# Kernel optimization log

Measured on AMD Instinct MI355X. Metric: run time of the kernel, lower is better.

Reference implementation:

```python
import jax, jax.numpy as jnp
import numpy as np

DEPTH, HEADS, DIM_HEAD = 6, 8, 64
B, N, E = 2, 128, 160
NUM_ATOMS, NF = 100, 127
DIM = NF + 1                 # 128, node feature dim fed to transformer
INNER = HEADS * DIM_HEAD     # 512


def setup_inputs() -> dict:
    key = jax.random.key(0)
    ks = iter(jax.random.split(key, 40))
    f32 = jnp.float32
    def w(shape, scale=0.02):
        return jax.random.normal(next(ks), shape, dtype=f32) * scale
    inp = {
        "indices": jax.random.randint(next(ks), (B, N), 0, NUM_ATOMS),
        "coordinates": jax.random.normal(next(ks), (B, N, 3), dtype=f32),
        "bonds": jax.random.randint(next(ks), (E, 2), 0, N),
        "noise_level": jax.random.uniform(next(ks), (1,), dtype=f32),
        "atom_emb": w((NUM_ATOMS, NF), 1.0),
        "ln1_g": jnp.ones((DEPTH, DIM), f32), "ln1_b": jnp.zeros((DEPTH, DIM), f32),
        "Wq": w((DEPTH, DIM, INNER)), "bq": jnp.zeros((DEPTH, INNER), f32),
        "Wkv": w((DEPTH, DIM, 2 * INNER)), "bkv": jnp.zeros((DEPTH, 2 * INNER), f32),
        "We": w((DEPTH, 3, INNER)), "be": jnp.zeros((DEPTH, INNER), f32),
        "Wo": w((DEPTH, INNER, DIM)), "bo": jnp.zeros((DEPTH, DIM), f32),
        "Wg1": w((DEPTH, 3 * DIM, 1)),
        "ln2_g": jnp.ones((DEPTH, DIM), f32), "ln2_b": jnp.zeros((DEPTH, DIM), f32),
        "W1": w((DEPTH, DIM, 4 * DIM)), "b1": jnp.zeros((DEPTH, 4 * DIM), f32),
        "W2": w((DEPTH, 4 * DIM, DIM)), "b2": jnp.zeros((DEPTH, DIM), f32),
        "Wg2": w((DEPTH, 3 * DIM, 1)),
        "Wlin": w((DIM, 1)), "blin": jnp.zeros((1,), f32),
    }
    return inp


def _ln(x, g, b, eps=1e-5):
    m = jnp.mean(x, -1, keepdims=True)
    v = jnp.mean((x - m) ** 2, -1, keepdims=True)
    return (x - m) * jax.lax.rsqrt(v + eps) * g + b


def _gated_residual(x, res, Wg):
    # gate = sigmoid(Linear([x, res, x-res])); out = x*gate + res*(1-gate)
    gate = jax.nn.sigmoid(jnp.concatenate([x, res, x - res], -1) @ Wg)  # (B,N,1)
    return x * gate + res * (1.0 - gate)


def _forward(indices, bonds, coordinates, noise_level, atom_emb,
             ln1_g, ln1_b, Wq, bq, Wkv, bkv, We, be, Wo, bo, Wg1,
             ln2_g, ln2_b, W1, b1, W2, b2, Wg2, Wlin, blin):
    b, n = indices.shape
    # nodes_embedding: atom embedding + noise-level channel
    noise = jnp.broadcast_to(noise_level.reshape(1, 1, 1).astype(coordinates.dtype), (b, n, 1))
    nodes = jnp.concatenate([atom_emb[indices], noise], -1)  # (B,N,DIM)
    # edges_embedding: vectorized scatter of per-bond coordinate differences
    i, j = bonds[:, 0], bonds[:, 1]
    diff = coordinates[:, i] - coordinates[:, j]             # (B,E,3)
    edges = jnp.zeros((b, n, n, 3), coordinates.dtype)
    edges = edges.at[:, i, j].set(diff).at[:, j, i].set(-diff)

    scale = DIM_HEAD ** -0.5
    for l in range(DEPTH):
        # PreNorm + edge-biased attention (mask is all-ones -> no-op)
        xn = _ln(nodes, ln1_g[l], ln1_b[l])
        q = (xn @ Wq[l] + bq[l]).reshape(b, n, HEADS, DIM_HEAD)
        k, v = jnp.split(xn @ Wkv[l] + bkv[l], 2, -1)
        k = k.reshape(b, n, HEADS, DIM_HEAD)
        v = v.reshape(b, n, HEADS, DIM_HEAD)
        e = (edges @ We[l] + be[l]).reshape(b, n, n, HEADS, DIM_HEAD)
        kk = k[:, None] + e                                   # (B,i,j,H,D)
        vv = v[:, None] + e
        sim = jnp.einsum('bihd,bijhd->bijh', q, kk) * scale
        attn = jax.nn.softmax(sim, axis=2)                    # softmax over j
        out = jnp.einsum('bijh,bijhd->bihd', attn, vv).reshape(b, n, INNER)
        out = out @ Wo[l] + bo[l]
        nodes = _gated_residual(out, nodes, Wg1[l])
        # PreNorm + FeedForward (exact GELU, mult=4) + gated residual
        xn = _ln(nodes, ln2_g[l], ln2_b[l])
        ff = jax.nn.gelu(xn @ W1[l] + b1[l], approximate=False) @ W2[l] + b2[l]
        nodes = _gated_residual(ff, nodes, Wg2[l])
    return jnp.sum(nodes @ Wlin + blin)


def reference(indices, coordinates, bonds, noise_level, atom_emb,
              ln1_g, ln1_b, Wq, bq, Wkv, bkv, We, be, Wo, bo, Wg1,
              ln2_g, ln2_b, W1, b1, W2, b2, Wg2, Wlin, blin):
    return _forward(indices, bonds, coordinates, noise_level, atom_emb,
                    ln1_g, ln1_b, Wq, bq, Wkv, bkv, We, be, Wo, bo, Wg1,
                    ln2_g, ln2_b, W1, b1, W2, b2, Wg2, Wlin, blin)
```

## Files before the change

### kernel.cpp

```cpp
#include <hip/hip_runtime.h>
#include <hip/hip_fp16.h>
#include <math.h>

#define DEPTH 6
#define HEADS 8
#define BB    2
#define NN    128
#define EE    160
#define NF    127
#define DIMM  128
#define INNER 512
#define NNODE 256

__device__ __forceinline__ void gload16(const void* g, void* l) {
    __builtin_amdgcn_global_load_lds((const __attribute__((address_space(1))) void*)g,
                                     (__attribute__((address_space(3))) void*)l,
                                     16, 0, 0);
}

__device__ __forceinline__ void wait_vm0() { __builtin_amdgcn_s_waitcnt(0x0f70); }
__device__ __forceinline__ void wait_lgkm0() { __builtin_amdgcn_s_waitcnt(0xC07F); }

__device__ __forceinline__ void wstage16(const char* gslice, char* ldsslice, int ln) {
#pragma unroll
    for (int i = 0; i < 16; i++)
        gload16(gslice + i * 1024 + ln * 16, ldsslice + i * 1024);
}
__device__ __forceinline__ void wstage16s(const char* gslice, int rowstride,
                                          char* ldsslice, int ln) {
#pragma unroll
    for (int i = 0; i < 16; i++)
        gload16(gslice + (size_t)i * rowstride + ln * 16, ldsslice + i * 1024);
}

__device__ __forceinline__ void fma8h(float4& a0, float4& a1, float s, float4 raw) {
    const __half2* hp = (const __half2*)&raw;
    float2 p0 = __half22float2(hp[0]), p1 = __half22float2(hp[1]);
    float2 p2 = __half22float2(hp[2]), p3 = __half22float2(hp[3]);
    a0.x += s * p0.x; a0.y += s * p0.y; a0.z += s * p1.x; a0.w += s * p1.y;
    a1.x += s * p2.x; a1.y += s * p2.y; a1.z += s * p3.x; a1.w += s * p3.y;
}

__device__ __forceinline__ void gemv512(const float* act, const float* wbuf,
                                        float* s_part, int w, int ln) {
    float4 a0 = {0,0,0,0}, a1 = {0,0,0,0};
    const float4* w4 = (const float4*)wbuf;
#pragma unroll
    for (int r = 0; r < 16; r++)
        fma8h(a0, a1, act[w * 16 + r], w4[r * 64 + ln]);
    ((float4*)(s_part + w * 512))[ln * 2]     = a0;
    ((float4*)(s_part + w * 512))[ln * 2 + 1] = a1;
}

__device__ __forceinline__ void gemv128(const float* act, const float* wbuf,
                                        float* s_part, int w, int ln) {
    float2 acc = {0, 0};
#pragma unroll 8
    for (int r = 0; r < 64; r++) {
        float raw = wbuf[r * 64 + ln];
        __half2 h = *(__half2*)&raw;
        float2 p = __half22float2(h);
        float a = act[w * 64 + r];
        acc.x += a * p.x; acc.y += a * p.y;
    }
    s_part[w * 128 + ln * 2]     = acc.x;
    s_part[w * 128 + ln * 2 + 1] = acc.y;
}

__device__ __forceinline__ float block_reduce_sum_8w(float val, float* sbuf) {
#pragma unroll
    for (int off = 32; off > 0; off >>= 1) val += __shfl_xor(val, off, 64);
    int wave = threadIdx.x >> 6;
    if ((threadIdx.x & 63) == 0) sbuf[wave] = val;
    __syncthreads();
    float r = sbuf[0] + sbuf[1] + sbuf[2] + sbuf[3] + sbuf[4] + sbuf[5] + sbuf[6] + sbuf[7];
    __syncthreads();
    return r;
}


__global__ __launch_bounds__(512) void k_cvt(const float* Wq, const float* Wkv,
                                             const float* Wo, const float* W1,
                                             const float* W2,
                                             __half* hWq, __half* hWkv, __half* hWo,
                                             __half* hW1, __half* hW2) {
    int g = blockIdx.x * 512 + threadIdx.x;
    const float4* src; __half* dst; int off;
    if (g < 98304)       { src = (const float4*)Wq;  dst = hWq;  off = g; }
    else if (g < 294912) { src = (const float4*)Wkv; dst = hWkv; off = g - 98304; }
    else if (g < 393216) { src = (const float4*)Wo;  dst = hWo;  off = g - 294912; }
    else if (g < 491520) { src = (const float4*)W1;  dst = hW1;  off = g - 393216; }
    else                 { src = (const float4*)W2;  dst = hW2;  off = g - 491520; }
    float4 v = src[off];
    __half2* d2 = (__half2*)(dst + (size_t)off * 4);
    d2[0] = __floats2half2_rn(v.x, v.y);
    d2[1] = __floats2half2_rn(v.z, v.w);
}

__global__ __launch_bounds__(512, 1) void k_pre(const int* indices, const float* noise,
                                                const float* atom_emb,
                                                const float* ln1_g, const float* ln1_b,
                                                const __half* hWq, const float* bq,
                                                const __half* hWkv, const float* bkv,
                                                float* nodes, float* qb,
                                                __half* hk, __half* hv) {
    int bn = blockIdx.x;
    int t  = threadIdx.x;
    int d  = t & 127;
    bool own = (t < 128);
    int w = t >> 6, ln = t & 63;
    __shared__ float arena[32768];
    __shared__ float s_xn[128];
    __shared__ float s_red[8];
    __shared__ float s_part[4096];
    char*  lslice = (char*)arena + w * 16384;
    float* wbuf   = arena + w * 4096;

    const char* WqL  = (const char*)(hWq + 0);
    const char* WkvL = (const char*)(hWkv + 0);
    wstage16(WqL + w * 16384, lslice, ln);

    float nd = 0.0f;
    if (own) {
        int idx = indices[bn];
        nd = (d < NF) ? atom_emb[idx * NF + d] : noise[0];
        nodes[bn * DIMM + d] = nd;
    }
    float m   = block_reduce_sum_8w(own ? nd : 0.0f, s_red) * (1.0f / 128.0f);
    float df  = nd - m;
    float var = block_reduce_sum_8w(own ? df * df : 0.0f, s_red) * (1.0f / 128.0f);
    if (own) s_xn[d] = df * rsqrtf(var + 1e-5f) * ln1_g[d] + ln1_b[d];
    __syncthreads();

    wait_vm0();
    gemv512(s_xn, wbuf, s_part, w, ln);
    wait_lgkm0();
    wstage16s(WkvL + (size_t)(w * 16) * 2048, 2048, lslice, ln);
    __syncthreads();
    {
        float q = bq[t];
#pragma unroll
        for (int g = 0; g < 8; g++) q += s_part[g * 512 + t];
        qb[(size_t)bn * INNER + t] = q;
    }
    __syncthreads();

    wait_vm0();
    gemv512(s_xn, wbuf, s_part, w, ln);
    wait_lgkm0();
    wstage16s(WkvL + (size_t)(w * 16) * 2048 + 1024, 2048, lslice, ln);
    __syncthreads();
    {
        float k = bkv[t];
#pragma unroll
        for (int g = 0; g < 8; g++) k += s_part[g * 512 + t];
        hk[(size_t)bn * INNER + t] = __float2half(k);
    }
    __syncthreads();

    wait_vm0();
    gemv512(s_xn, wbuf, s_part, w, ln);
    __syncthreads();
    {
        float v = bkv[INNER + t];
#pragma unroll
        for (int g = 0; g < 8; g++) v += s_part[g * 512 + t];
        hv[(size_t)bn * INNER + t] = __float2half(v);
    }
}

__global__ __launch_bounds__(512, 1) void k_layer(int l,
        const float* coords, const int* bonds,
        const float* We, const float* be,
        float* qb, const __half* hkin, const __half* hvin,
        __half* hkout, __half* hvout,
        const __half* hWo, const float* bo, const float* Wg1,
        const float* ln2_g, const float* ln2_b,
        const __half* hW1, const float* b1,
        const __half* hW2, const float* b2,
        const float* Wg2,
        const float* ln1_g, const float* ln1_b,
        const __half* hWq, const float* bq,
        const __half* hWkv, const float* bkv,
        float* nodes) {
    int bn = blockIdx.x;
    int b = bn >> 7, i = bn & 127;
    int t = threadIdx.x;
    int d = t & 127;
    bool own = (t < 128);
    int w = t >> 6, ln = t & 63;

    __shared__ float arena[32768];
    __shared__ float scoord[384];
    __shared__ float sedge[384];
    __shared__ int   sadj[128];
    __shared__ float s_l[32];
    __shared__ float s_ao[512];
    __shared__ float s_h[512];
    __shared__ float s_xn[128];
    __shared__ float s_red[8];
    __shared__ float s_part[4096];
    float* s_o = s_part;
    char*  lslice = (char*)arena + w * 16384;
    float* wbuf   = arena + w * 4096;

    const char* WoL  = (const char*)(hWo + (size_t)l * INNER * DIMM);
    const char* W1L  = (const char*)(hW1 + (size_t)l * DIMM * 4 * DIMM);
    const char* W2L  = (const char*)(hW2 + (size_t)l * 4 * DIMM * DIMM);
    const char* WqL  = (const char*)(hWq + (size_t)(l + 1) * DIMM * INNER);
    const char* WkvL = (const char*)(hWkv + (size_t)(l + 1) * DIMM * 2 * INNER);

    wstage16(WoL + w * 16384, lslice, ln);

    int jg = t >> 7, c = t & 127, h = c >> 4;
    const float4* qR  = (const float4*)(qb + (size_t)bn * INNER);
    const float4* WeR = (const float4*)(We + (size_t)l * 3 * INNER);
    float4 qv  = qR[c];
    float4 we0 = WeR[c], we1 = WeR[128 + c], we2 = WeR[256 + c];
    float4 bev = ((const float4*)(be + (size_t)l * INNER))[c];
    float res = own ? nodes[bn * DIMM + d] : 0.0f;

    if (t < 3 * NN) scoord[t] = coords[b * 3 * NN + t];
    if (t < NN) sadj[t] = 0;
    __syncthreads();
    if (t < EE) {
        int e0 = bonds[2 * t], e1 = bonds[2 * t + 1];
        if (e0 == i) sadj[e1] = 1;
        if (e1 == i) sadj[e0] = 1;
    }
    __syncthreads();
    if (t < NN) {
        int j = t;
        float msk = sadj[j] ? 1.0f : 0.0f;
        sedge[3 * j + 0] = msk * (scoord[3 * i + 0] - scoord[3 * j + 0]);
        sedge[3 * j + 1] = msk * (scoord[3 * i + 1] - scoord[3 * j + 1]);
        sedge[3 * j + 2] = msk * (scoord[3 * i + 2] - scoord[3 * j + 2]);
    }
    __syncthreads();

    const float2* kR2 = (const float2*)(hkin + (size_t)b * NN * INNER);
    const float2* vR2 = (const float2*)(hvin + (size_t)b * NN * INNER);
    float l_run = 0.0f;
    float4 o_run = {0, 0, 0, 0};
    int j0 = jg * 32;
#pragma unroll
    for (int base = 0; base < 32; base += 8) {
        float2 kraw[8], vraw[8];
#pragma unroll
        for (int p = 0; p < 8; p++) {
            int j = j0 + base + p;
            kraw[p] = kR2[j * 128 + c];
            vraw[p] = vR2[j * 128 + c];
        }
#pragma unroll
        for (int p = 0; p < 8; p++) {
            int j = j0 + base + p;
            float ex = sedge[3 * j], ey = sedge[3 * j + 1], ez = sedge[3 * j + 2];
            float4 e;
            e.x = bev.x + ex * we0.x + ey * we1.x + ez * we2.x;
            e.y = bev.y + ex * we0.y + ey * we1.y + ez * we2.y;
            e.z = bev.z + ex * we0.z + ey * we1.z + ez * we2.z;
            e.w = bev.w + ex * we0.w + ey * we1.w + ez * we2.w;
            const __half2* kh = (const __half2*)&kraw[p];
            float2 k01 = __half22float2(kh[0]), k23 = __half22float2(kh[1]);
            float s = (qv.x * (k01.x + e.x) + qv.y * (k01.y + e.y))
                    + (qv.z * (k23.x + e.z) + qv.w * (k23.y + e.w));
            s += __shfl_xor(s, 1, 64);
            s += __shfl_xor(s, 2, 64);
            s += __shfl_xor(s, 4, 64);
            s += __shfl_xor(s, 8, 64);
            float pp = __expf(s * 0.125f);
            const __half2* vh = (const __half2*)&vraw[p];
            float2 v01 = __half22float2(vh[0]), v23 = __half22float2(vh[1]);
            l_run += pp;
            o_run.x += pp * (v01.x + e.x);
            o_run.y += pp * (v01.y + e.y);
            o_run.z += pp * (v23.x + e.z);
            o_run.w += pp * (v23.y + e.w);
        }
    }
    ((float4*)(s_o + jg * INNER))[c] = o_run;
    if ((c & 15) == 0) s_l[jg * HEADS + h] = l_run;
    __syncthreads();
    if (jg == 0) {
        float4 o = o_run;
        float lsum = l_run;
#pragma unroll
        for (int g = 1; g < 4; g++) {
            float4 og = ((float4*)(s_o + g * INNER))[c];
            o.x += og.x; o.y += og.y; o.z += og.z; o.w += og.w;
            lsum += s_l[g * HEADS + h];
        }
        float inv = 1.0f / lsum;
        float4 rr; rr.x = o.x * inv; rr.y = o.y * inv; rr.z = o.z * inv; rr.w = o.w * inv;
        ((float4*)s_ao)[c] = rr;
    }
    __syncthreads();

    wait_vm0();
    gemv128(s_ao, wbuf, s_part, w, ln);
    wait_lgkm0();
    wstage16(W1L + w * 16384, lslice, ln);
    __syncthreads();
    float x = 0.0f;
    if (own) {
        x = bo[l * DIMM + d];
#pragma unroll
        for (int g = 0; g < 8; g++) x += s_part[g * 128 + d];
    }
    __syncthreads();

    const float* Wg1_l = Wg1 + l * 3 * DIMM;
    float texpr = own ? (x * Wg1_l[d] + res * Wg1_l[DIMM + d] + (x - res) * Wg1_l[2 * DIMM + d]) : 0.0f;
    float g1 = block_reduce_sum_8w(texpr, s_red);
    g1 = 1.0f / (1.0f + __expf(-g1));
    float n1 = x * g1 + res * (1.0f - g1);

    float m   = block_reduce_sum_8w(own ? n1 : 0.0f, s_red) * (1.0f / 128.0f);
    float df  = n1 - m;
    float var = block_reduce_sum_8w(own ? df * df : 0.0f, s_red) * (1.0f / 128.0f);
    if (own) s_xn[d] = df * rsqrtf(var + 1e-5f) * ln2_g[l * DIMM + d] + ln2_b[l * DIMM + d];
    __syncthreads();

    wait_vm0();
    gemv512(s_xn, wbuf, s_part, w, ln);
    wait_lgkm0();
    wstage16(W2L + w * 16384, lslice, ln);
    __syncthreads();
    {
        float a = b1[l * 4 * DIMM + t];
#pragma unroll
        for (int g = 0; g < 8; g++) a += s_part[g * 512 + t];
        a = 0.5f * a * (1.0f + erff(a * 0.70710678f));
        s_h[t] = a;
    }
    __syncthreads();

    wait_vm0();
    gemv128(s_h, wbuf, s_part, w, ln);
    wait_lgkm0();
    if (l < DEPTH - 1) wstage16(WqL + w * 16384, lslice, ln);
    __syncthreads();
    float y = 0.0f;
    if (own) {
        y = b2[l * DIMM + d];
#pragma unroll
        for (int g = 0; g < 8; g++) y += s_part[g * 128 + d];
    }
    __syncthreads();

    const float* Wg2_l = Wg2 + l * 3 * DIMM;
    texpr = own ? (y * Wg2_l[d] + n1 * Wg2_l[DIMM + d] + (y - n1) * Wg2_l[2 * DIMM + d]) : 0.0f;
    float g2 = block_reduce_sum_8w(texpr, s_red);
    g2 = 1.0f / (1.0f + __expf(-g2));
    float n2 = y * g2 + n1 * (1.0f - g2);
    if (own) nodes[bn * DIMM + d] = n2;

    if (l < DEPTH - 1) {
        float m1   = block_reduce_sum_8w(own ? n2 : 0.0f, s_red) * (1.0f / 128.0f);
        float df1  = n2 - m1;
        float var1 = block_reduce_sum_8w(own ? df1 * df1 : 0.0f, s_red) * (1.0f / 128.0f);
        if (own) s_xn[d] = df1 * rsqrtf(var1 + 1e-5f) * ln1_g[(l + 1) * DIMM + d]
                         + ln1_b[(l + 1) * DIMM + d];
        __syncthreads();

        wait_vm0();
        gemv512(s_xn, wbuf, s_part, w, ln);
        wait_lgkm0();
        wstage16s(WkvL + (size_t)(w * 16) * 2048, 2048, lslice, ln);
        __syncthreads();
        {
            float q = bq[(l + 1) * INNER + t];
#pragma unroll
            for (int g = 0; g < 8; g++) q += s_part[g * 512 + t];
            qb[(size_t)bn * INNER + t] = q;
        }
        __syncthreads();

        wait_vm0();
        gemv512(s_xn, wbuf, s_part, w, ln);
        wait_lgkm0();
        wstage16s(WkvL + (size_t)(w * 16) * 2048 + 1024, 2048, lslice, ln);
        __syncthreads();
        {
            float k = bkv[(l + 1) * 2 * INNER + t];
#pragma unroll
            for (int g = 0; g < 8; g++) k += s_part[g * 512 + t];
            hkout[(size_t)bn * INNER + t] = __float2half(k);
        }
        __syncthreads();

        wait_vm0();
        gemv512(s_xn, wbuf, s_part, w, ln);
        __syncthreads();
        {
            float v = bkv[(l + 1) * 2 * INNER + INNER + t];
#pragma unroll
            for (int g = 0; g < 8; g++) v += s_part[g * 512 + t];
            hvout[(size_t)bn * INNER + t] = __float2half(v);
        }
    }
}

__global__ __launch_bounds__(256) void k_final(const float* nodes, const float* Wlin,
                                               const float* blin, float* out) {
    int t = threadIdx.x;
    __shared__ float s_w[DIMM];
    if (t < DIMM) s_w[t] = Wlin[t];
    __syncthreads();
    float s = blin[0];
    const float4* nr = (const float4*)(nodes + t * DIMM);
#pragma unroll 8
    for (int q = 0; q < 32; q++) {
        float4 n = nr[q];
        s += n.x * s_w[4 * q] + n.y * s_w[4 * q + 1] + n.z * s_w[4 * q + 2] + n.w * s_w[4 * q + 3];
    }
#pragma unroll
    for (int off = 32; off > 0; off >>= 1) s += __shfl_xor(s, off, 64);
    __shared__ float sb[4];
    int wave = t >> 6, lane = t & 63;
    if (lane == 0) sb[wave] = s;
    __syncthreads();
    if (t == 0) out[0] = sb[0] + sb[1] + sb[2] + sb[3];
}

extern "C" void kernel_launch(void* const* d_in, const int* in_sizes, int n_in,
                              void* d_out, int out_size, void* d_ws, size_t ws_size,
                              hipStream_t stream) {
    const int*   indices = (const int*)d_in[0];
    const float* coords  = (const float*)d_in[1];
    const int*   bonds   = (const int*)d_in[2];
    const float* noise   = (const float*)d_in[3];
    const float* atom_emb= (const float*)d_in[4];
    const float* ln1_g   = (const float*)d_in[5];
    const float* ln1_b   = (const float*)d_in[6];
    const float* Wq      = (const float*)d_in[7];
    const float* bq      = (const float*)d_in[8];
    const float* Wkv     = (const float*)d_in[9];
    const float* bkv     = (const float*)d_in[10];
    const float* We      = (const float*)d_in[11];
    const float* be      = (const float*)d_in[12];
    const float* Wo      = (const float*)d_in[13];
    const float* bo      = (const float*)d_in[14];
    const float* Wg1     = (const float*)d_in[15];
    const float* ln2_g   = (const float*)d_in[16];
    const float* ln2_b   = (const float*)d_in[17];
    const float* W1      = (const float*)d_in[18];
    const float* b1      = (const float*)d_in[19];
    const float* W2      = (const float*)d_in[20];
    const float* b2      = (const float*)d_in[21];
    const float* Wg2     = (const float*)d_in[22];
    const float* Wlin    = (const float*)d_in[23];
    const float* blin    = (const float*)d_in[24];

    float*  ws    = (float*)d_ws;
    float*  nodes = ws;
    float*  qb    = nodes + NNODE * DIMM;
    __half* hkb   = (__half*)(qb + NNODE * INNER);
    __half* hvb   = hkb + 2 * NNODE * INNER;
    __half* hWq   = hvb + 2 * NNODE * INNER;
    __half* hWkv  = hWq + DEPTH * DIMM * INNER;
    __half* hWo   = hWkv + DEPTH * DIMM * 2 * INNER;
    __half* hW1   = hWo + DEPTH * INNER * DIMM;
    __half* hW2   = hW1 + DEPTH * DIMM * 4 * DIMM;

    k_cvt<<<1152, 512, 0, stream>>>(Wq, Wkv, Wo, W1, W2, hWq, hWkv, hWo, hW1, hW2);
    k_pre<<<NNODE, 512, 0, stream>>>(indices, noise, atom_emb, ln1_g, ln1_b,
                                     hWq, bq, hWkv, bkv, nodes, qb, hkb, hvb);
    for (int l = 0; l < DEPTH; l++) {
        const __half* hkin = hkb + (size_t)(l & 1) * NNODE * INNER;
        const __half* hvin = hvb + (size_t)(l & 1) * NNODE * INNER;
        __half* hkout = hkb + (size_t)((l + 1) & 1) * NNODE * INNER;
        __half* hvout = hvb + (size_t)((l + 1) & 1) * NNODE * INNER;
        k_layer<<<NNODE, 512, 0, stream>>>(l, coords, bonds, We, be,
                                           qb, hkin, hvin, hkout, hvout,
                                           hWo, bo, Wg1, ln2_g, ln2_b, hW1, b1, hW2, b2,
                                           Wg2, ln1_g, ln1_b, hWq, bq, hWkv, bkv, nodes);
    }
    k_final<<<1, 256, 0, stream>>>(nodes, Wlin, blin, (float*)d_out);
}
```

Measured before the change: 281.9 us.

## Fuse final projection into last layer, merge LayerNorm reductions, repartition attention

```diff
diff --git a/kernel.cpp b/kernel.cpp
--- a/kernel.cpp
+++ b/kernel.cpp
@@ -78,12 +78,31 @@
     return r;
 }
 
+__device__ __forceinline__ float2 block_reduce_sum2_8w(float a, float b, float* sbuf16) {
+#pragma unroll
+    for (int off = 32; off > 0; off >>= 1) {
+        a += __shfl_xor(a, off, 64);
+        b += __shfl_xor(b, off, 64);
+    }
+    int wave = threadIdx.x >> 6;
+    if ((threadIdx.x & 63) == 0) { sbuf16[2 * wave] = a; sbuf16[2 * wave + 1] = b; }
+    __syncthreads();
+    float ra = 0.0f, rb = 0.0f;
+#pragma unroll
+    for (int g = 0; g < 8; g++) { ra += sbuf16[2 * g]; rb += sbuf16[2 * g + 1]; }
+    __syncthreads();
+    float2 r; r.x = ra; r.y = rb;
+    return r;
+}
+
 
 __global__ __launch_bounds__(512) void k_cvt(const float* Wq, const float* Wkv,
                                              const float* Wo, const float* W1,
                                              const float* W2,
                                              __half* hWq, __half* hWkv, __half* hWo,
-                                             __half* hW1, __half* hW2) {
+                                             __half* hW1, __half* hW2,
+                                             const float* blin, float* out) {
+    if (blockIdx.x == 0 && threadIdx.x == 0) out[0] = 256.0f * blin[0];
     int g = blockIdx.x * 512 + threadIdx.x;
     const float4* src; __half* dst; int off;
     if (g < 98304)       { src = (const float4*)Wq;  dst = hWq;  off = g; }
@@ -111,7 +130,7 @@
     int w = t >> 6, ln = t & 63;
     __shared__ float arena[32768];
     __shared__ float s_xn[128];
-    __shared__ float s_red[8];
+    __shared__ float s_red[16];
     __shared__ float s_part[4096];
     char*  lslice = (char*)arena + w * 16384;
     float* wbuf   = arena + w * 4096;
@@ -126,10 +145,10 @@
         nd = (d < NF) ? atom_emb[idx * NF + d] : noise[0];
         nodes[bn * DIMM + d] = nd;
     }
-    float m   = block_reduce_sum_8w(own ? nd : 0.0f, s_red) * (1.0f / 128.0f);
-    float df  = nd - m;
-    float var = block_reduce_sum_8w(own ? df * df : 0.0f, s_red) * (1.0f / 128.0f);
-    if (own) s_xn[d] = df * rsqrtf(var + 1e-5f) * ln1_g[d] + ln1_b[d];
+    float2 ss = block_reduce_sum2_8w(own ? nd : 0.0f, own ? nd * nd : 0.0f, s_red);
+    float m   = ss.x * (1.0f / 128.0f);
+    float var = ss.y * (1.0f / 128.0f) - m * m;
+    if (own) s_xn[d] = (nd - m) * rsqrtf(var + 1e-5f) * ln1_g[d] + ln1_b[d];
     __syncthreads();
 
     wait_vm0();
@@ -182,7 +201,7 @@
         const float* ln1_g, const float* ln1_b,
         const __half* hWq, const float* bq,
         const __half* hWkv, const float* bkv,
-        float* nodes) {
+        float* nodes, const float* Wlin, float* out) {
     int bn = blockIdx.x;
     int b = bn >> 7, i = bn & 127;
     int t = threadIdx.x;
@@ -194,11 +213,11 @@
     __shared__ float scoord[384];
     __shared__ float sedge[384];
     __shared__ int   sadj[128];
-    __shared__ float s_l[32];
+    __shared__ float s_l[64];
     __shared__ float s_ao[512];
     __shared__ float s_h[512];
     __shared__ float s_xn[128];
-    __shared__ float s_red[8];
+    __shared__ float s_red[16];
     __shared__ float s_part[4096];
     float* s_o = s_part;
     char*  lslice = (char*)arena + w * 16384;
@@ -212,12 +231,14 @@
 
     wstage16(WoL + w * 16384, lslice, ln);
 
-    int jg = t >> 7, c = t & 127, h = c >> 4;
-    const float4* qR  = (const float4*)(qb + (size_t)bn * INNER);
+    const float4* qR4 = (const float4*)(qb + (size_t)bn * INNER);
     const float4* WeR = (const float4*)(We + (size_t)l * 3 * INNER);
-    float4 qv  = qR[c];
-    float4 we0 = WeR[c], we1 = WeR[128 + c], we2 = WeR[256 + c];
-    float4 bev = ((const float4*)(be + (size_t)l * INNER))[c];
+    float4 qa  = qR4[ln * 2],        qz  = qR4[ln * 2 + 1];
+    float4 w0a = WeR[ln * 2],        w0z = WeR[ln * 2 + 1];
+    float4 w1a = WeR[128 + ln * 2],  w1z = WeR[129 + ln * 2];
+    float4 w2a = WeR[256 + ln * 2],  w2z = WeR[257 + ln * 2];
+    float4 bea = ((const float4*)(be + (size_t)l * INNER))[ln * 2];
+    float4 bez = ((const float4*)(be + (size_t)l * INNER))[ln * 2 + 1];
     float res = own ? nodes[bn * DIMM + d] : 0.0f;
 
     if (t < 3 * NN) scoord[t] = coords[b * 3 * NN + t];
@@ -238,62 +259,67 @@
     }
     __syncthreads();
 
-    const float2* kR2 = (const float2*)(hkin + (size_t)b * NN * INNER);
-    const float2* vR2 = (const float2*)(hvin + (size_t)b * NN * INNER);
+    const float4* kR = (const float4*)(hkin + (size_t)b * NN * INNER);
+    const float4* vR = (const float4*)(hvin + (size_t)b * NN * INNER);
     float l_run = 0.0f;
-    float4 o_run = {0, 0, 0, 0};
-    int j0 = jg * 32;
-#pragma unroll
-    for (int base = 0; base < 32; base += 8) {
-        float2 kraw[8], vraw[8];
-#pragma unroll
-        for (int p = 0; p < 8; p++) {
+    float4 o0 = {0, 0, 0, 0}, o1 = {0, 0, 0, 0};
+    int j0 = w * 16;
+#pragma unroll
+    for (int base = 0; base < 16; base += 4) {
+        float4 kraw[4], vraw[4];
+#pragma unroll
+        for (int p = 0; p < 4; p++) {
             int j = j0 + base + p;
-            kraw[p] = kR2[j * 128 + c];
-            vraw[p] = vR2[j * 128 + c];
+            kraw[p] = kR[j * 64 + ln];
+            vraw[p] = vR[j * 64 + ln];
         }
 #pragma unroll
-        for (int p = 0; p < 8; p++) {
+        for (int p = 0; p < 4; p++) {
             int j = j0 + base + p;
             float ex = sedge[3 * j], ey = sedge[3 * j + 1], ez = sedge[3 * j + 2];
-            float4 e;
-            e.x = bev.x + ex * we0.x + ey * we1.x + ez * we2.x;
-            e.y = bev.y + ex * we0.y + ey * we1.y + ez * we2.y;
-            e.z = bev.z + ex * we0.z + ey * we1.z + ez * we2.z;
-            e.w = bev.w + ex * we0.w + ey * we1.w + ez * we2.w;
+            float4 e0, e1;
+            e0.x = bea.x + ex * w0a.x + ey * w1a.x + ez * w2a.x;
+            e0.y = bea.y + ex * w0a.y + ey * w1a.y + ez * w2a.y;
+            e0.z = bea.z + ex * w0a.z + ey * w1a.z + ez * w2a.z;
+            e0.w = bea.w + ex * w0a.w + ey * w1a.w + ez * w2a.w;
+            e1.x = bez.x + ex * w0z.x + ey * w1z.x + ez * w2z.x;
+            e1.y = bez.y + ex * w0z.y + ey * w1z.y + ez * w2z.y;
+            e1.z = bez.z + ex * w0z.z + ey * w1z.z + ez * w2z.z;
+            e1.w = bez.w + ex * w0z.w + ey * w1z.w + ez * w2z.w;
             const __half2* kh = (const __half2*)&kraw[p];
-            float2 k01 = __half22float2(kh[0]), k23 = __half22float2(kh[1]);
-            float s = (qv.x * (k01.x + e.x) + qv.y * (k01.y + e.y))
-                    + (qv.z * (k23.x + e.z) + qv.w * (k23.y + e.w));
+            float2 k0 = __half22float2(kh[0]), k1 = __half22float2(kh[1]);
+            float2 k2 = __half22float2(kh[2]), k3 = __half22float2(kh[3]);
+            float s = qa.x * (k0.x + e0.x) + qa.y * (k0.y + e0.y)
+                    + qa.z * (k1.x + e0.z) + qa.w * (k1.y + e0.w)
+                    + qz.x * (k2.x + e1.x) + qz.y * (k2.y + e1.y)
+                    + qz.z * (k3.x + e1.z) + qz.w * (k3.y + e1.w);
             s += __shfl_xor(s, 1, 64);
             s += __shfl_xor(s, 2, 64);
             s += __shfl_xor(s, 4, 64);
-            s += __shfl_xor(s, 8, 64);
             float pp = __expf(s * 0.125f);
             const __half2* vh = (const __half2*)&vraw[p];
-            float2 v01 = __half22float2(vh[0]), v23 = __half22float2(vh[1]);
+            float2 v0 = __half22float2(vh[0]), v1 = __half22float2(vh[1]);
+            float2 v2 = __half22float2(vh[2]), v3 = __half22float2(vh[3]);
             l_run += pp;
-            o_run.x += pp * (v01.x + e.x);
-            o_run.y += pp * (v01.y + e.y);
-            o_run.z += pp * (v23.x + e.z);
-            o_run.w += pp * (v23.y + e.w);
+            o0.x += pp * (v0.x + e0.x); o0.y += pp * (v0.y + e0.y);
+            o0.z += pp * (v1.x + e0.z); o0.w += pp * (v1.y + e0.w);
+            o1.x += pp * (v2.x + e1.x); o1.y += pp * (v2.y + e1.y);
+            o1.z += pp * (v3.x + e1.z); o1.w += pp * (v3.y + e1.w);
         }
     }
-    ((float4*)(s_o + jg * INNER))[c] = o_run;
-    if ((c & 15) == 0) s_l[jg * HEADS + h] = l_run;
-    __syncthreads();
-    if (jg == 0) {
-        float4 o = o_run;
-        float lsum = l_run;
-#pragma unroll
-        for (int g = 1; g < 4; g++) {
-            float4 og = ((float4*)(s_o + g * INNER))[c];
-            o.x += og.x; o.y += og.y; o.z += og.z; o.w += og.w;
-            lsum += s_l[g * HEADS + h];
-        }
-        float inv = 1.0f / lsum;
-        float4 rr; rr.x = o.x * inv; rr.y = o.y * inv; rr.z = o.z * inv; rr.w = o.w * inv;
-        ((float4*)s_ao)[c] = rr;
+    ((float4*)(s_o + w * 512))[ln * 2]     = o0;
+    ((float4*)(s_o + w * 512))[ln * 2 + 1] = o1;
+    if ((ln & 7) == 0) s_l[w * 8 + (ln >> 3)] = l_run;
+    __syncthreads();
+    {
+        float o = 0.0f;
+#pragma unroll
+        for (int g = 0; g < 8; g++) o += s_o[g * 512 + t];
+        int h = t >> 6;
+        float lsum = 0.0f;
+#pragma unroll
+        for (int g = 0; g < 8; g++) lsum += s_l[g * 8 + h];
+        s_ao[t] = o / lsum;
     }
     __syncthreads();
 
@@ -316,10 +342,10 @@
     g1 = 1.0f / (1.0f + __expf(-g1));
     float n1 = x * g1 + res * (1.0f - g1);
 
-    float m   = block_reduce_sum_8w(own ? n1 : 0.0f, s_red) * (1.0f / 128.0f);
-    float df  = n1 - m;
-    float var = block_reduce_sum_8w(own ? df * df : 0.0f, s_red) * (1.0f / 128.0f);
-    if (own) s_xn[d] = df * rsqrtf(var + 1e-5f) * ln2_g[l * DIMM + d] + ln2_b[l * DIMM + d];
+    float2 ss = block_reduce_sum2_8w(own ? n1 : 0.0f, own ? n1 * n1 : 0.0f, s_red);
+    float m   = ss.x * (1.0f / 128.0f);
+    float var = ss.y * (1.0f / 128.0f) - m * m;
+    if (own) s_xn[d] = (n1 - m) * rsqrtf(var + 1e-5f) * ln2_g[l * DIMM + d] + ln2_b[l * DIMM + d];
     __syncthreads();
 
     wait_vm0();
@@ -357,10 +383,10 @@
     if (own) nodes[bn * DIMM + d] = n2;
 
     if (l < DEPTH - 1) {
-        float m1   = block_reduce_sum_8w(own ? n2 : 0.0f, s_red) * (1.0f / 128.0f);
-        float df1  = n2 - m1;
-        float var1 = block_reduce_sum_8w(own ? df1 * df1 : 0.0f, s_red) * (1.0f / 128.0f);
-        if (own) s_xn[d] = df1 * rsqrtf(var1 + 1e-5f) * ln1_g[(l + 1) * DIMM + d]
+        float2 s1 = block_reduce_sum2_8w(own ? n2 : 0.0f, own ? n2 * n2 : 0.0f, s_red);
+        float m1   = s1.x * (1.0f / 128.0f);
+        float var1 = s1.y * (1.0f / 128.0f) - m1 * m1;
+        if (own) s_xn[d] = (n2 - m1) * rsqrtf(var1 + 1e-5f) * ln1_g[(l + 1) * DIMM + d]
                          + ln1_b[(l + 1) * DIMM + d];
         __syncthreads();
 
@@ -399,29 +425,11 @@
             for (int g = 0; g < 8; g++) v += s_part[g * 512 + t];
             hvout[(size_t)bn * INNER + t] = __float2half(v);
         }
-    }
-}
-
-__global__ __launch_bounds__(256) void k_final(const float* nodes, const float* Wlin,
-                                               const float* blin, float* out) {
-    int t = threadIdx.x;
-    __shared__ float s_w[DIMM];
-    if (t < DIMM) s_w[t] = Wlin[t];
-    __syncthreads();
-    float s = blin[0];
-    const float4* nr = (const float4*)(nodes + t * DIMM);
-#pragma unroll 8
-    for (int q = 0; q < 32; q++) {
-        float4 n = nr[q];
-        s += n.x * s_w[4 * q] + n.y * s_w[4 * q + 1] + n.z * s_w[4 * q + 2] + n.w * s_w[4 * q + 3];
-    }
-#pragma unroll
-    for (int off = 32; off > 0; off >>= 1) s += __shfl_xor(s, off, 64);
-    __shared__ float sb[4];
-    int wave = t >> 6, lane = t & 63;
-    if (lane == 0) sb[wave] = s;
-    __syncthreads();
-    if (t == 0) out[0] = sb[0] + sb[1] + sb[2] + sb[3];
+    } else {
+        float contrib = own ? n2 * Wlin[d] : 0.0f;
+        float tot = block_reduce_sum_8w(contrib, s_red);
+        if (t == 0) atomicAdd(out, tot);
+    }
 }
 
 extern "C" void kernel_launch(void* const* d_in, const int* in_sizes, int n_in,
@@ -464,7 +472,8 @@
     __half* hW1   = hWo + DEPTH * INNER * DIMM;
     __half* hW2   = hW1 + DEPTH * DIMM * 4 * DIMM;
 
-    k_cvt<<<1152, 512, 0, stream>>>(Wq, Wkv, Wo, W1, W2, hWq, hWkv, hWo, hW1, hW2);
+    k_cvt<<<1152, 512, 0, stream>>>(Wq, Wkv, Wo, W1, W2, hWq, hWkv, hWo, hW1, hW2,
+                                    blin, (float*)d_out);
     k_pre<<<NNODE, 512, 0, stream>>>(indices, noise, atom_emb, ln1_g, ln1_b,
                                      hWq, bq, hWkv, bkv, nodes, qb, hkb, hvb);
     for (int l = 0; l < DEPTH; l++) {
@@ -475,7 +484,7 @@
         k_layer<<<NNODE, 512, 0, stream>>>(l, coords, bonds, We, be,
                                            qb, hkin, hvin, hkout, hvout,
                                            hWo, bo, Wg1, ln2_g, ln2_b, hW1, b1, hW2, b2,
-                                           Wg2, ln1_g, ln1_b, hWq, bq, hWkv, bkv, nodes);
-    }
-    k_final<<<1, 256, 0, stream>>>(nodes, Wlin, blin, (float*)d_out);
-}
+                                           Wg2, ln1_g, ln1_b, hWq, bq, hWkv, bkv,
+                                           nodes, Wlin, (float*)d_out);
+    }
+}
```

After: 267.0 us. 1.06x faster.
